# Kernel optimization log

Measured on AMD Instinct MI355X. Metric: run time of the kernel, lower is better.

Reference implementation:

```python
import jax, jax.numpy as jnp
import numpy as np

NUM_HEADS = 16


def setup_inputs() -> dict:
    key = jax.random.key(0)
    ks = jax.random.split(key, 7)
    B, S, D = 2, 2048, 1024
    return {
        "query": jax.random.normal(ks[0], (B, S, D), jnp.float32),
        "key": jax.random.normal(ks[1], (B, S, D), jnp.float32),
        "value": jax.random.normal(ks[2], (B, S, D), jnp.float32),
        "qk_w": jax.random.normal(ks[3], (2 * D, D), jnp.float32) * (D ** -0.5),
        "qk_b": jax.random.normal(ks[4], (2 * D,), jnp.float32) * 0.02,
        "out_w": jax.random.normal(ks[5], (D, D), jnp.float32) * (D ** -0.5),
        "out_b": jax.random.normal(ks[6], (D,), jnp.float32) * 0.02,
    }


def reference(query, key, value, qk_w, qk_b, out_w, out_b):
    # Hand-rolled multi-head attention with fused QK projection (both Q and K
    # come from `query`); `key` arg is unused (as in the source forward).
    B, S, D = query.shape
    H = NUM_HEADS
    dh = D // H
    scale = D ** -0.5  # source uses d_model**-0.5, not head_dim

    qk = query @ qk_w.T + qk_b                      # [B, S, 2D]
    qk = qk.reshape(B, S, 2, H, dh).transpose(2, 0, 3, 1, 4)  # [2, B, H, S, dh]
    q, k = qk[0], qk[1]                              # [B, H, S, dh]

    scores = jnp.einsum("bhqd,bhkd->bhqk", q, k) * scale  # [B, H, S, S]
    attn = jax.nn.softmax(scores, axis=-1)
    # dropout_p = 0.0 -> identity (eval mode)

    v = value.reshape(B, S, H, dh).transpose(0, 2, 1, 3)   # [B, H, S, dh]
    out = jnp.einsum("bhqk,bhkd->bhqd", attn, v)           # [B, H, S, dh]
    out = out.transpose(0, 2, 1, 3).reshape(B, S, D)       # merge heads
    return out @ out_w.T + out_b
```

## Files before the change

### kernel.cpp

```cpp
#include <hip/hip_runtime.h>
#include <hip/hip_bf16.h>
#include <stdint.h>

typedef __attribute__((ext_vector_type(8))) short bf16x8;
typedef __attribute__((ext_vector_type(4))) short bf16x4;
typedef __attribute__((ext_vector_type(4))) float f32x4;
typedef __attribute__((ext_vector_type(16))) float f32x16;

#define B_ 2
#define H_ 16
#define S_ 2048
#define D_ 1024
#define DH 64

__device__ __forceinline__ void gload_lds16(const void* g, void* l) {
  __builtin_amdgcn_global_load_lds((const __attribute__((address_space(1))) void*)g,
                                   (__attribute__((address_space(3))) void*)l, 16, 0, 0);
}

__device__ __forceinline__ float exp2_hw(float x) {
  float r;
  asm("v_exp_f32 %0, %1" : "=v"(r) : "v"(x));
  return r;
}

__device__ __forceinline__ uint32_t packbf2(float lo, float hi) {
  union { __hip_bfloat162 h; uint32_t u; } u;
  u.h = __float22bfloat162_rn(make_float2(lo, hi));
  return u.u;
}

__device__ __forceinline__ void pl32swap(uint32_t& a, uint32_t& b) {
  asm volatile("v_permlane32_swap_b32 %0, %1" : "+v"(a), "+v"(b));
}

__global__ void k_f2b3(const float* __restrict__ a, __hip_bfloat16* __restrict__ da,
                       const float* __restrict__ b, __hip_bfloat16* __restrict__ db,
                       const float* __restrict__ c, __hip_bfloat16* __restrict__ dc) {
  int i = blockIdx.x * blockDim.x + threadIdx.x;
  const float* src;
  __hip_bfloat16* dst;
  int off;
  if (i < 524288) { src = a; dst = da; off = i; }
  else if (i < 786432) { src = b; dst = db; off = i - 524288; }
  else { src = c; dst = dc; off = i - 786432; }
  const float4* p = (const float4*)src + (size_t)off * 2;
  float4 x = p[0], y = p[1];
  union { bf16x8 v; __hip_bfloat16 h[8]; } u;
  u.h[0] = __float2bfloat16(x.x); u.h[1] = __float2bfloat16(x.y);
  u.h[2] = __float2bfloat16(x.z); u.h[3] = __float2bfloat16(x.w);
  u.h[4] = __float2bfloat16(y.x); u.h[5] = __float2bfloat16(y.y);
  u.h[6] = __float2bfloat16(y.z); u.h[7] = __float2bfloat16(y.w);
  *((bf16x8*)dst + off) = u.v;
}

__global__ void k_vt(const float* __restrict__ v, __hip_bfloat16* __restrict__ vt) {
  __shared__ float tile[64][65];
  const int bh = blockIdx.y, b = bh >> 4, h = bh & 15;
  const int s0 = blockIdx.x * 64;
  const int t = threadIdx.x;
#pragma unroll
  for (int it = 0; it < 4; ++it) {
    const int r = it * 16 + (t >> 4);
    const int c = (t & 15) * 4;
    const float4 x = *(const float4*)(v + (size_t)(b * S_ + s0 + r) * D_ + h * DH + c);
    tile[r][c] = x.x; tile[r][c + 1] = x.y; tile[r][c + 2] = x.z; tile[r][c + 3] = x.w;
  }
  __syncthreads();
#pragma unroll
  for (int it = 0; it < 4; ++it) {
    const int d = it * 16 + (t >> 4);
    const int j = (t & 15) * 4;
    union { bf16x4 v4; __hip_bfloat16 e[4]; } u;
    u.e[0] = __float2bfloat16(tile[j][d]);
    u.e[1] = __float2bfloat16(tile[j + 1][d]);
    u.e[2] = __float2bfloat16(tile[j + 2][d]);
    u.e[3] = __float2bfloat16(tile[j + 3][d]);
    *(bf16x4*)(vt + (size_t)(bh * DH + d) * S_ + s0 + j) = u.v4;
  }
}

__device__ __forceinline__ void gemm_core(
    const __hip_bfloat16* __restrict__ A, const __hip_bfloat16* __restrict__ Bm,
    int m0, int n0, __hip_bfloat16* As, __hip_bfloat16* Bs, f32x4 acc[4][4]) {
  const int t = threadIdx.x;
  const int l = t & 63, w = t >> 6;
  const int wr = w >> 1, wc = w & 1;
  const int lr = l & 15, lc = l >> 4;
  const int slot = (t & 7) ^ ((t >> 3) & 7);
  const int r0 = t >> 3;
  const __hip_bfloat16* gA = A + (size_t)(m0 + r0) * 1024 + slot * 8;
  const __hip_bfloat16* gB = Bm + (size_t)(n0 + r0) * 1024 + slot * 8;
  char* AsB = (char*)As;
  char* BsB = (char*)Bs;

#define GSTAGE(bi, k0)                                               \
  {                                                                  \
    char* la = AsB + (bi) * 16384 + t * 16;                          \
    char* lb = BsB + (bi) * 16384 + t * 16;                          \
    _Pragma("unroll") for (int c = 0; c < 4; ++c) {                  \
      gload_lds16(gA + (size_t)(c * 32) * 1024 + (k0), la + c * 4096); \
      gload_lds16(gB + (size_t)(c * 32) * 1024 + (k0), lb + c * 4096); \
    }                                                                \
  }

  GSTAGE(0, 0)
  __syncthreads();
  int buf = 0;
  for (int it = 0; it < 16; ++it) {
    if (it < 15) GSTAGE(buf ^ 1, (it + 1) * 64)
    const char* ab = AsB + buf * 16384;
    const char* bb = BsB + buf * 16384;
#pragma unroll
    for (int kk = 0; kk < 2; ++kk) {
      bf16x8 af[4], bv[4];
#pragma unroll
      for (int i = 0; i < 4; ++i) {
        const int r = wr * 64 + i * 16 + lr;
        af[i] = *(const bf16x8*)(ab + r * 128 + (((kk * 4 + lc) ^ (r & 7)) << 4));
      }
#pragma unroll
      for (int j = 0; j < 4; ++j) {
        const int r = wc * 64 + j * 16 + lr;
        bv[j] = *(const bf16x8*)(bb + r * 128 + (((kk * 4 + lc) ^ (r & 7)) << 4));
      }
#pragma unroll
      for (int i = 0; i < 4; ++i)
#pragma unroll
        for (int j = 0; j < 4; ++j)
          acc[i][j] = __builtin_amdgcn_mfma_f32_16x16x32_bf16(af[i], bv[j], acc[i][j], 0, 0, 0);
    }
    __syncthreads();
    buf ^= 1;
  }
#undef GSTAGE
}

__global__ __launch_bounds__(256) void k_gemm_qk(
    const __hip_bfloat16* __restrict__ A, const __hip_bfloat16* __restrict__ Bm,
    const float* __restrict__ bias,
    __hip_bfloat16* __restrict__ Qh, __hip_bfloat16* __restrict__ Kh) {
  __shared__ __align__(16) __hip_bfloat16 As[2][128 * 64];
  __shared__ __align__(16) __hip_bfloat16 Bs[2][128 * 64];
  f32x4 acc[4][4] = {};
  const int m0 = blockIdx.x * 128, n0 = blockIdx.y * 128;
  gemm_core(A, Bm, m0, n0, &As[0][0], &Bs[0][0], acc);
  const int t = threadIdx.x, l = t & 63, w = t >> 6;
  const int wr = w >> 1, wc = w & 1, lr = l & 15, lc = l >> 4;
#pragma unroll
  for (int j = 0; j < 4; ++j) {
    const int col = n0 + wc * 64 + j * 16 + lr;
    const float bv = bias[col];
    const int inK = col >> 10;
    const int hh = (col & 1023) >> 6, dd = col & 63;
    __hip_bfloat16* dst = inK ? Kh : Qh;
    const float sc = inK ? 1.0f : 0.045084220f;
#pragma unroll
    for (int i = 0; i < 4; ++i) {
#pragma unroll
      for (int r = 0; r < 4; ++r) {
        const int row = m0 + wr * 64 + i * 16 + lc * 4 + r;
        const int b = row >> 11, s = row & 2047;
        const float vv = (acc[i][j][r] + bv) * sc;
        dst[((size_t)(b * H_ + hh) * S_ + s) * DH + dd] = __float2bfloat16(vv);
      }
    }
  }
}

__global__ __launch_bounds__(256) void k_gemm_out(
    const __hip_bfloat16* __restrict__ A, const __hip_bfloat16* __restrict__ Bm,
    const float* __restrict__ bias, float* __restrict__ out) {
  __shared__ __align__(16) __hip_bfloat16 As[2][128 * 64];
  __shared__ __align__(16) __hip_bfloat16 Bs[2][128 * 64];
  f32x4 acc[4][4] = {};
  const int m0 = blockIdx.x * 128, n0 = blockIdx.y * 128;
  gemm_core(A, Bm, m0, n0, &As[0][0], &Bs[0][0], acc);
  const int t = threadIdx.x, l = t & 63, w = t >> 6;
  const int wr = w >> 1, wc = w & 1, lr = l & 15, lc = l >> 4;
#pragma unroll
  for (int j = 0; j < 4; ++j) {
    const int col = n0 + wc * 64 + j * 16 + lr;
    const float bv = bias[col];
#pragma unroll
    for (int i = 0; i < 4; ++i) {
#pragma unroll
      for (int r = 0; r < 4; ++r) {
        const int row = m0 + wr * 64 + i * 16 + lc * 4 + r;
        out[(size_t)row * D_ + col] = acc[i][j][r] + bv;
      }
    }
  }
}

__global__ __launch_bounds__(256, 4) void k_attn(
    const __hip_bfloat16* __restrict__ Qh, const __hip_bfloat16* __restrict__ Kh,
    const __hip_bfloat16* __restrict__ VT,
    __hip_bfloat16* __restrict__ pO0, __hip_bfloat16* __restrict__ pO1,
    float* __restrict__ l0a, float* __restrict__ l1a) {
  __shared__ __align__(16) __hip_bfloat16 KV[2][8192];
  const int bh = blockIdx.y, q0 = blockIdx.x * 128;
  const int half = blockIdx.z;
  const int jbeg = half << 10, jend = jbeg + 1024;
  const int t = threadIdx.x, l = t & 63, w = t >> 6;
  const int qi = l & 31, hi = l >> 5;
  const __hip_bfloat16* Qb = Qh + (size_t)bh * S_ * DH;
  const __hip_bfloat16* Kb = Kh + (size_t)bh * S_ * DH;
  const __hip_bfloat16* Vb = VT + (size_t)bh * DH * S_;

  bf16x8 qf[4];
#pragma unroll
  for (int dc = 0; dc < 4; ++dc)
    qf[dc] = *(const bf16x8*)&Qb[(size_t)(q0 + w * 32 + qi) * DH + dc * 16 + hi * 8];

  const int tr = t >> 4, tc = t & 15;
  const int c0 = tc ^ (tr & 15);
  const int c1 = tc ^ ((tr + 16) & 15);
  const __hip_bfloat16* gK0 = Kb + (size_t)(tr + (c0 >= 8 ? 32 : 0)) * DH + (c0 & 7) * 8;
  const __hip_bfloat16* gK1 = Kb + (size_t)(tr + 16 + (c1 >= 8 ? 32 : 0)) * DH + (c1 & 7) * 8;
  const __hip_bfloat16* gV0 = Vb + (size_t)(tr + (c0 >= 8 ? 32 : 0)) * S_ + (c0 & 7) * 8;
  const __hip_bfloat16* gV1 = Vb + (size_t)(tr + 16 + (c1 >= 8 ? 32 : 0)) * S_ + (c1 & 7) * 8;

#define STAGE(bufi, j0)                                              \
  {                                                                  \
    __hip_bfloat16* Ld = &KV[bufi][0];                               \
    gload_lds16(gK0 + (size_t)(j0) * DH, Ld + t * 8);                \
    gload_lds16(gK1 + (size_t)(j0) * DH, Ld + 2048 + t * 8);         \
    gload_lds16(gV0 + (j0), Ld + 4096 + t * 8);                      \
    gload_lds16(gV1 + (j0), Ld + 4096 + 2048 + t * 8);               \
  }

  f32x16 oacc0 = {}, oacc1 = {};
  float lsum = 0.f;
  int buf = 0;

  STAGE(0, jbeg)
  __syncthreads();

  const int rsw = (qi & 15) << 4;

  for (int j0 = jbeg; j0 < jend; j0 += 64) {
    if (j0 + 64 < jend) STAGE(buf ^ 1, j0 + 64)
    const char* KsB = (const char*)&KV[buf][0];
    const char* VsB = (const char*)&KV[buf][4096];

    f32x16 s0 = {}, s1 = {};
    __builtin_amdgcn_s_setprio(1);
#pragma unroll
    for (int dc = 0; dc < 4; ++dc) {
      const int cb = dc * 32 + hi * 16;
      const bf16x8 kf0 = *(const bf16x8*)(KsB + qi * 256 + (cb ^ rsw));
      const bf16x8 kf1 = *(const bf16x8*)(KsB + qi * 256 + ((128 + cb) ^ rsw));
      s0 = __builtin_amdgcn_mfma_f32_32x32x16_bf16(kf0, qf[dc], s0, 0, 0, 0);
      s1 = __builtin_amdgcn_mfma_f32_32x32x16_bf16(kf1, qf[dc], s1, 0, 0, 0);
    }
    __builtin_amdgcn_s_setprio(0);

#pragma unroll
    for (int r = 0; r < 16; ++r) s0[r] = exp2_hw(s0[r]);
#pragma unroll
    for (int r = 0; r < 16; ++r) s1[r] = exp2_hw(s1[r]);
    float ts[16];
#pragma unroll
    for (int r = 0; r < 16; ++r) ts[r] = s0[r] + s1[r];
#pragma unroll
    for (int st = 8; st > 0; st >>= 1)
#pragma unroll
      for (int r = 0; r < st; ++r) ts[r] += ts[r + st];
    lsum += ts[0] + __shfl_xor(ts[0], 32, 64);

#define PVSTEP(SS, KSOFF)                                                         \
  {                                                                               \
    uint32_t w0 = packbf2(SS[0], SS[1]), w1 = packbf2(SS[2], SS[3]);              \
    uint32_t w2 = packbf2(SS[4], SS[5]), w3 = packbf2(SS[6], SS[7]);              \
    uint32_t w4 = packbf2(SS[8], SS[9]), w5 = packbf2(SS[10], SS[11]);            \
    uint32_t w6 = packbf2(SS[12], SS[13]), w7 = packbf2(SS[14], SS[15]);          \
    pl32swap(w0, w2); pl32swap(w1, w3); pl32swap(w4, w6); pl32swap(w5, w7);       \
    union { bf16x8 v; uint32_t u[4]; } pa0, pa1;                                  \
    pa0.u[0] = w0; pa0.u[1] = w1; pa0.u[2] = w2; pa0.u[3] = w3;                   \
    pa1.u[0] = w4; pa1.u[1] = w5; pa1.u[2] = w6; pa1.u[3] = w7;                   \
    const int cb = (KSOFF) + hi * 16;                                             \
    bf16x8 vf;                                                                    \
    vf = *(const bf16x8*)(VsB + qi * 256 + ((cb + 0) ^ rsw));                     \
    oacc0 = __builtin_amdgcn_mfma_f32_32x32x16_bf16(pa0.v, vf, oacc0, 0, 0, 0);   \
    vf = *(const bf16x8*)(VsB + qi * 256 + ((cb + 32) ^ rsw));                    \
    oacc0 = __builtin_amdgcn_mfma_f32_32x32x16_bf16(pa1.v, vf, oacc0, 0, 0, 0);   \
    vf = *(const bf16x8*)(VsB + qi * 256 + ((cb + 128) ^ rsw));                   \
    oacc1 = __builtin_amdgcn_mfma_f32_32x32x16_bf16(pa0.v, vf, oacc1, 0, 0, 0);   \
    vf = *(const bf16x8*)(VsB + qi * 256 + ((cb + 128 + 32) ^ rsw));              \
    oacc1 = __builtin_amdgcn_mfma_f32_32x32x16_bf16(pa1.v, vf, oacc1, 0, 0, 0);   \
  }
    __builtin_amdgcn_s_setprio(1);
    PVSTEP(s0, 0)
    PVSTEP(s1, 64)
    __builtin_amdgcn_s_setprio(0);

    __syncthreads();
    buf ^= 1;
  }

  __hip_bfloat16* pO = half ? pO1 : pO0;
  float* la = half ? l1a : l0a;
  const size_t rowb = (size_t)bh * S_ + q0 + w * 32;
#pragma unroll
  for (int r = 0; r < 16; ++r) {
    const int qloc = (r & 3) + 8 * (r >> 2) + 4 * hi;
    pO[(rowb + qloc) * 64 + qi] = __float2bfloat16(oacc0[r]);
    pO[(rowb + qloc) * 64 + 32 + qi] = __float2bfloat16(oacc1[r]);
  }
  if (l < 32) la[rowb + qi] = lsum;
#undef STAGE
#undef PVSTEP
}

__global__ __launch_bounds__(256) void k_combine(
    const __hip_bfloat16* __restrict__ pO0, const __hip_bfloat16* __restrict__ pO1,
    const float* __restrict__ l0a, const float* __restrict__ l1a,
    __hip_bfloat16* __restrict__ aO) {
  const int tid = blockIdx.x * 256 + threadIdx.x;
  const float inv = 1.0f / (l0a[tid] + l1a[tid]);
  const bf16x8* r0 = (const bf16x8*)(pO0 + (size_t)tid * 64);
  const bf16x8* r1 = (const bf16x8*)(pO1 + (size_t)tid * 64);
  const int bh = tid >> 11, s = tid & 2047, bb = bh >> 4, h = bh & 15;
  __hip_bfloat16* o = aO + ((size_t)(bb * S_ + s)) * D_ + h * DH;
#pragma unroll
  for (int j = 0; j < 8; ++j) {
    union { bf16x8 v; __hip_bfloat16 e[8]; } v0, v1, u;
    v0.v = r0[j]; v1.v = r1[j];
#pragma unroll
    for (int e = 0; e < 8; ++e)
      u.e[e] = __float2bfloat16(inv * (__bfloat162float(v0.e[e]) + __bfloat162float(v1.e[e])));
    *(bf16x8*)(o + j * 8) = u.v;
  }
}

extern "C" void kernel_launch(void* const* d_in, const int* in_sizes, int n_in,
                              void* d_out, int out_size, void* d_ws, size_t ws_size,
                              hipStream_t stream) {
  const float* q   = (const float*)d_in[0];
  const float* val = (const float*)d_in[2];
  const float* qkw = (const float*)d_in[3];
  const float* qkb = (const float*)d_in[4];
  const float* ow  = (const float*)d_in[5];
  const float* ob  = (const float*)d_in[6];
  float* out = (float*)d_out;

  __hip_bfloat16* ws  = (__hip_bfloat16*)d_ws;
  __hip_bfloat16* qA  = ws;
  __hip_bfloat16* w1b = qA + 4194304;
  __hip_bfloat16* w2b = w1b + 2097152;
  __hip_bfloat16* Qh  = w2b + 1048576;
  __hip_bfloat16* Kh  = Qh + 4194304;
  __hip_bfloat16* VT  = Kh + 4194304;
  __hip_bfloat16* aO  = VT + 4194304;
  __hip_bfloat16* pO1 = aO + 4194304;
  __hip_bfloat16* pO0 = qA;
  float* l0a = (float*)w1b;
  float* l1a = l0a + 65536;

  hipLaunchKernelGGL(k_f2b3, dim3(3584), dim3(256), 0, stream, q, qA, qkw, w1b, ow, w2b);
  hipLaunchKernelGGL(k_vt, dim3(32, 32), dim3(256), 0, stream, val, VT);
  hipLaunchKernelGGL(k_gemm_qk, dim3(32, 16), dim3(256), 0, stream, qA, w1b, qkb, Qh, Kh);
  hipLaunchKernelGGL(k_attn, dim3(16, 32, 2), dim3(256), 0, stream, Qh, Kh, VT, pO0, pO1, l0a, l1a);
  hipLaunchKernelGGL(k_combine, dim3(256), dim3(256), 0, stream, pO0, pO1, l0a, l1a, aO);
  hipLaunchKernelGGL(k_gemm_out, dim3(32, 8), dim3(256), 0, stream, aO, w2b, ob, out);
}
```

Before: 121.6 us.

## Merge prep kernels, shrink GEMM K-tile to 32, halve out-GEMM N-tile

Fuses the fp32-to-bf16 conversion and the V transpose into one launch, removing a kernel launch. The shared GEMM core moves from 64-wide to 32-wide K stages with a new XOR swizzle, halving LDS per block to allow more resident blocks at the cost of twice as many barriers. The output projection GEMM is specialized to 128x64 tiles, doubling its grid to 512 blocks for better CU coverage, in exchange for less operand reuse per block.

```diff
diff --git a/kernel.cpp b/kernel.cpp
--- a/kernel.cpp
+++ b/kernel.cpp
@@ -34,37 +34,40 @@
   asm volatile("v_permlane32_swap_b32 %0, %1" : "+v"(a), "+v"(b));
 }
 
-__global__ void k_f2b3(const float* __restrict__ a, __hip_bfloat16* __restrict__ da,
+__global__ void k_prep(const float* __restrict__ a, __hip_bfloat16* __restrict__ da,
                        const float* __restrict__ b, __hip_bfloat16* __restrict__ db,
-                       const float* __restrict__ c, __hip_bfloat16* __restrict__ dc) {
-  int i = blockIdx.x * blockDim.x + threadIdx.x;
-  const float* src;
-  __hip_bfloat16* dst;
-  int off;
-  if (i < 524288) { src = a; dst = da; off = i; }
-  else if (i < 786432) { src = b; dst = db; off = i - 524288; }
-  else { src = c; dst = dc; off = i - 786432; }
-  const float4* p = (const float4*)src + (size_t)off * 2;
-  float4 x = p[0], y = p[1];
-  union { bf16x8 v; __hip_bfloat16 h[8]; } u;
-  u.h[0] = __float2bfloat16(x.x); u.h[1] = __float2bfloat16(x.y);
-  u.h[2] = __float2bfloat16(x.z); u.h[3] = __float2bfloat16(x.w);
-  u.h[4] = __float2bfloat16(y.x); u.h[5] = __float2bfloat16(y.y);
-  u.h[6] = __float2bfloat16(y.z); u.h[7] = __float2bfloat16(y.w);
-  *((bf16x8*)dst + off) = u.v;
-}
-
-__global__ void k_vt(const float* __restrict__ v, __hip_bfloat16* __restrict__ vt) {
+                       const float* __restrict__ c, __hip_bfloat16* __restrict__ dc,
+                       const float* __restrict__ v, __hip_bfloat16* __restrict__ vt) {
   __shared__ float tile[64][65];
-  const int bh = blockIdx.y, b = bh >> 4, h = bh & 15;
-  const int s0 = blockIdx.x * 64;
+  const int bid = blockIdx.x;
   const int t = threadIdx.x;
+  if (bid < 3584) {
+    int i = bid * 256 + t;
+    const float* src;
+    __hip_bfloat16* dst;
+    int off;
+    if (i < 524288) { src = a; dst = da; off = i; }
+    else if (i < 786432) { src = b; dst = db; off = i - 524288; }
+    else { src = c; dst = dc; off = i - 786432; }
+    const float4* p = (const float4*)src + (size_t)off * 2;
+    float4 x = p[0], y = p[1];
+    union { bf16x8 v8; __hip_bfloat16 h[8]; } u;
+    u.h[0] = __float2bfloat16(x.x); u.h[1] = __float2bfloat16(x.y);
+    u.h[2] = __float2bfloat16(x.z); u.h[3] = __float2bfloat16(x.w);
+    u.h[4] = __float2bfloat16(y.x); u.h[5] = __float2bfloat16(y.y);
+    u.h[6] = __float2bfloat16(y.z); u.h[7] = __float2bfloat16(y.w);
+    *((bf16x8*)dst + off) = u.v8;
+    return;
+  }
+  const int vid = bid - 3584;
+  const int bh = vid >> 5, bb = bh >> 4, h = bh & 15;
+  const int s0 = (vid & 31) * 64;
 #pragma unroll
   for (int it = 0; it < 4; ++it) {
     const int r = it * 16 + (t >> 4);
-    const int c = (t & 15) * 4;
-    const float4 x = *(const float4*)(v + (size_t)(b * S_ + s0 + r) * D_ + h * DH + c);
-    tile[r][c] = x.x; tile[r][c + 1] = x.y; tile[r][c + 2] = x.z; tile[r][c + 3] = x.w;
+    const int cc = (t & 15) * 4;
+    const float4 x = *(const float4*)(v + (size_t)(bb * S_ + s0 + r) * D_ + h * DH + cc);
+    tile[r][cc] = x.x; tile[r][cc + 1] = x.y; tile[r][cc + 2] = x.z; tile[r][cc + 3] = x.w;
   }
   __syncthreads();
 #pragma unroll
@@ -87,61 +90,55 @@
   const int l = t & 63, w = t >> 6;
   const int wr = w >> 1, wc = w & 1;
   const int lr = l & 15, lc = l >> 4;
-  const int slot = (t & 7) ^ ((t >> 3) & 7);
-  const int r0 = t >> 3;
-  const __hip_bfloat16* gA = A + (size_t)(m0 + r0) * 1024 + slot * 8;
-  const __hip_bfloat16* gB = Bm + (size_t)(n0 + r0) * 1024 + slot * 8;
-  char* AsB = (char*)As;
-  char* BsB = (char*)Bs;
-
-#define GSTAGE(bi, k0)                                               \
-  {                                                                  \
-    char* la = AsB + (bi) * 16384 + t * 16;                          \
-    char* lb = BsB + (bi) * 16384 + t * 16;                          \
-    _Pragma("unroll") for (int c = 0; c < 4; ++c) {                  \
-      gload_lds16(gA + (size_t)(c * 32) * 1024 + (k0), la + c * 4096); \
-      gload_lds16(gB + (size_t)(c * 32) * 1024 + (k0), lb + c * 4096); \
-    }                                                                \
-  }
-
-  GSTAGE(0, 0)
+  const int srow = t >> 2;
+  const int sbyte = ((t & 3) << 4) ^ ((srow & 3) << 4);
+  const char* AsB = (const char*)As;
+  const char* BsB = (const char*)Bs;
+  const int aswz = (lc << 4) ^ ((lr & 3) << 4);
+  const __hip_bfloat16* gA0 = A + (size_t)(m0 + srow) * 1024 + (sbyte >> 1);
+  const __hip_bfloat16* gB0 = Bm + (size_t)(n0 + srow) * 1024 + (sbyte >> 1);
+
+#define GSTAGE1(bi, k0)                                                 \
+  {                                                                     \
+    __hip_bfloat16* la = As + (bi) * 4096;                              \
+    __hip_bfloat16* lb = Bs + (bi) * 4096;                              \
+    gload_lds16(gA0 + (k0), la + t * 8);                                \
+    gload_lds16(gA0 + (size_t)64 * 1024 + (k0), la + (256 + t) * 8);    \
+    gload_lds16(gB0 + (k0), lb + t * 8);                                \
+    gload_lds16(gB0 + (size_t)64 * 1024 + (k0), lb + (256 + t) * 8);    \
+  }
+
+  GSTAGE1(0, 0)
   __syncthreads();
   int buf = 0;
-  for (int it = 0; it < 16; ++it) {
-    if (it < 15) GSTAGE(buf ^ 1, (it + 1) * 64)
-    const char* ab = AsB + buf * 16384;
-    const char* bb = BsB + buf * 16384;
-#pragma unroll
-    for (int kk = 0; kk < 2; ++kk) {
-      bf16x8 af[4], bv[4];
-#pragma unroll
-      for (int i = 0; i < 4; ++i) {
-        const int r = wr * 64 + i * 16 + lr;
-        af[i] = *(const bf16x8*)(ab + r * 128 + (((kk * 4 + lc) ^ (r & 7)) << 4));
-      }
-#pragma unroll
-      for (int j = 0; j < 4; ++j) {
-        const int r = wc * 64 + j * 16 + lr;
-        bv[j] = *(const bf16x8*)(bb + r * 128 + (((kk * 4 + lc) ^ (r & 7)) << 4));
-      }
-#pragma unroll
-      for (int i = 0; i < 4; ++i)
-#pragma unroll
-        for (int j = 0; j < 4; ++j)
-          acc[i][j] = __builtin_amdgcn_mfma_f32_16x16x32_bf16(af[i], bv[j], acc[i][j], 0, 0, 0);
-    }
+  for (int it = 0; it < 32; ++it) {
+    if (it < 31) GSTAGE1(buf ^ 1, (it + 1) * 32)
+    const char* ab = AsB + buf * 8192;
+    const char* bb = BsB + buf * 8192;
+    bf16x8 af[4], bv[4];
+#pragma unroll
+    for (int i = 0; i < 4; ++i)
+      af[i] = *(const bf16x8*)(ab + (wr * 64 + i * 16 + lr) * 64 + aswz);
+#pragma unroll
+    for (int j = 0; j < 4; ++j)
+      bv[j] = *(const bf16x8*)(bb + (wc * 64 + j * 16 + lr) * 64 + aswz);
+#pragma unroll
+    for (int i = 0; i < 4; ++i)
+#pragma unroll
+      for (int j = 0; j < 4; ++j)
+        acc[i][j] = __builtin_amdgcn_mfma_f32_16x16x32_bf16(af[i], bv[j], acc[i][j], 0, 0, 0);
     __syncthreads();
     buf ^= 1;
   }
-#undef GSTAGE
+#undef GSTAGE1
 }
 
 __global__ __launch_bounds__(256) void k_gemm_qk(
     const __hip_bfloat16* __restrict__ A, const __hip_bfloat16* __restrict__ Bm,
     const float* __restrict__ bias,
     __hip_bfloat16* __restrict__ Qh, __hip_bfloat16* __restrict__ Kh) {
-  __shared__ __align__(16) __hip_bfloat16 As[2][128 * 64];
-  __shared__ __align__(16) __hip_bfloat16 Bs[2][128 * 64];
+  __shared__ __align__(16) __hip_bfloat16 As[2][128 * 32];
+  __shared__ __align__(16) __hip_bfloat16 Bs[2][128 * 32];
   f32x4 acc[4][4] = {};
   const int m0 = blockIdx.x * 128, n0 = blockIdx.y * 128;
   gemm_core(A, Bm, m0, n0, &As[0][0], &Bs[0][0], acc);
@@ -171,23 +168,63 @@
 __global__ __launch_bounds__(256) void k_gemm_out(
     const __hip_bfloat16* __restrict__ A, const __hip_bfloat16* __restrict__ Bm,
     const float* __restrict__ bias, float* __restrict__ out) {
-  __shared__ __align__(16) __hip_bfloat16 As[2][128 * 64];
-  __shared__ __align__(16) __hip_bfloat16 Bs[2][128 * 64];
-  f32x4 acc[4][4] = {};
-  const int m0 = blockIdx.x * 128, n0 = blockIdx.y * 128;
-  gemm_core(A, Bm, m0, n0, &As[0][0], &Bs[0][0], acc);
-  const int t = threadIdx.x, l = t & 63, w = t >> 6;
-  const int wr = w >> 1, wc = w & 1, lr = l & 15, lc = l >> 4;
-#pragma unroll
-  for (int j = 0; j < 4; ++j) {
-    const int col = n0 + wc * 64 + j * 16 + lr;
-    const float bv = bias[col];
+  __shared__ __align__(16) __hip_bfloat16 As[2][128 * 32];
+  __shared__ __align__(16) __hip_bfloat16 Bs[2][64 * 32];
+  f32x4 acc[4][2] = {};
+  const int m0 = blockIdx.x * 128, n0 = blockIdx.y * 64;
+  const int t = threadIdx.x;
+  const int l = t & 63, w = t >> 6;
+  const int wr = w >> 1, wc = w & 1;
+  const int lr = l & 15, lc = l >> 4;
+  const int srow = t >> 2;
+  const int sbyte = ((t & 3) << 4) ^ ((srow & 3) << 4);
+  const char* AsB = (const char*)&As[0][0];
+  const char* BsB = (const char*)&Bs[0][0];
+  const int aswz = (lc << 4) ^ ((lr & 3) << 4);
+  const __hip_bfloat16* gA0 = A + (size_t)(m0 + srow) * 1024 + (sbyte >> 1);
+  const __hip_bfloat16* gB0 = Bm + (size_t)(n0 + srow) * 1024 + (sbyte >> 1);
+
+#define GSTAGE2(bi, k0)                                                   \
+  {                                                                       \
+    __hip_bfloat16* la = &As[bi][0];                                      \
+    gload_lds16(gA0 + (k0), la + t * 8);                                  \
+    gload_lds16(gA0 + (size_t)64 * 1024 + (k0), la + (256 + t) * 8);      \
+    gload_lds16(gB0 + (k0), &Bs[bi][0] + t * 8);                          \
+  }
+
+  GSTAGE2(0, 0)
+  __syncthreads();
+  int buf = 0;
+  for (int it = 0; it < 32; ++it) {
+    if (it < 31) GSTAGE2(buf ^ 1, (it + 1) * 32)
+    const char* ab = AsB + buf * 8192;
+    const char* bb = BsB + buf * 4096;
+    bf16x8 af[4], bv[2];
+#pragma unroll
+    for (int i = 0; i < 4; ++i)
+      af[i] = *(const bf16x8*)(ab + (wr * 64 + i * 16 + lr) * 64 + aswz);
+#pragma unroll
+    for (int j = 0; j < 2; ++j)
+      bv[j] = *(const bf16x8*)(bb + (wc * 32 + j * 16 + lr) * 64 + aswz);
+#pragma unroll
+    for (int i = 0; i < 4; ++i)
+#pragma unroll
+      for (int j = 0; j < 2; ++j)
+        acc[i][j] = __builtin_amdgcn_mfma_f32_16x16x32_bf16(af[i], bv[j], acc[i][j], 0, 0, 0);
+    __syncthreads();
+    buf ^= 1;
+  }
+#undef GSTAGE2
+#pragma unroll
+  for (int j = 0; j < 2; ++j) {
+    const int col = n0 + wc * 32 + j * 16 + lr;
+    const float bvv = bias[col];
 #pragma unroll
     for (int i = 0; i < 4; ++i) {
 #pragma unroll
       for (int r = 0; r < 4; ++r) {
         const int row = m0 + wr * 64 + i * 16 + lc * 4 + r;
-        out[(size_t)row * D_ + col] = acc[i][j][r] + bv;
+        out[(size_t)row * D_ + col] = acc[i][j][r] + bvv;
       }
     }
   }
@@ -358,10 +395,9 @@
   float* l0a = (float*)w1b;
   float* l1a = l0a + 65536;
 
-  hipLaunchKernelGGL(k_f2b3, dim3(3584), dim3(256), 0, stream, q, qA, qkw, w1b, ow, w2b);
-  hipLaunchKernelGGL(k_vt, dim3(32, 32), dim3(256), 0, stream, val, VT);
+  hipLaunchKernelGGL(k_prep, dim3(4608), dim3(256), 0, stream, q, qA, qkw, w1b, ow, w2b, val, VT);
   hipLaunchKernelGGL(k_gemm_qk, dim3(32, 16), dim3(256), 0, stream, qA, w1b, qkb, Qh, Kh);
   hipLaunchKernelGGL(k_attn, dim3(16, 32, 2), dim3(256), 0, stream, Qh, Kh, VT, pO0, pO1, l0a, l1a);
   hipLaunchKernelGGL(k_combine, dim3(256), dim3(256), 0, stream, pO0, pO1, l0a, l1a, aO);
-  hipLaunchKernelGGL(k_gemm_out, dim3(32, 8), dim3(256), 0, stream, aO, w2b, ob, out);
-}
+  hipLaunchKernelGGL(k_gemm_out, dim3(32, 16), dim3(256), 0, stream, aO, w2b, ob, out);
+}
```

After: 123.4 us. Within noise of the previous version (+1.4%).
